# Kernel optimization log

Hardware: AMD Instinct MI355X
Metric: run time of the kernel (lower is better)

Reference implementation:

```python
import jax, jax.numpy as jnp
import numpy as np

# YOLOv2 COCO anchors (w, h) in cell units
ANCHORS = np.array([[0.57273, 0.677385],
                    [1.87446, 2.06253],
                    [3.33843, 5.47434],
                    [7.88282, 3.52778],
                    [9.77052, 9.16828]], dtype=np.float32)

N, S, A, C = 16, 52, 5, 80
L_XY, L_WH, L_OBJ, L_NOOBJ, L_CLS = 5.0, 5.0, 1.0, 0.5, 1.0


def setup_inputs() -> dict:
    key = jax.random.key(0)
    k1, k2 = jax.random.split(key)
    pred = jax.random.normal(k1, (N, S, S, A, 5 + C), dtype=jnp.float32)
    target = jax.random.uniform(k2, (N, S, S, A, 5 + C), dtype=jnp.float32)
    return {"pred": pred, "target": target}


def _pairwise_iou(g, p):
    # g: [..., Agt, 4] gt boxes (cx, cy, w, h); p: [..., Apred, 4]
    g = g[..., :, None, :]   # [..., Agt, 1, 4]
    p = p[..., None, :, :]   # [..., 1, Apred, 4]
    g_x1, g_y1 = g[..., 0] - g[..., 2] / 2, g[..., 1] - g[..., 3] / 2
    g_x2, g_y2 = g[..., 0] + g[..., 2] / 2, g[..., 1] + g[..., 3] / 2
    p_x1, p_y1 = p[..., 0] - p[..., 2] / 2, p[..., 1] - p[..., 3] / 2
    p_x2, p_y2 = p[..., 0] + p[..., 2] / 2, p[..., 1] + p[..., 3] / 2
    iw = jnp.clip(jnp.minimum(g_x2, p_x2) - jnp.maximum(g_x1, p_x1), 0)
    ih = jnp.clip(jnp.minimum(g_y2, p_y2) - jnp.maximum(g_y1, p_y1), 0)
    inter = iw * ih
    union = (g_x2 - g_x1) * (g_y2 - g_y1) + (p_x2 - p_x1) * (p_y2 - p_y1) - inter + 1e-9
    return inter / union  # [..., Agt, Apred]


def reference(pred, target):
    anchors = jnp.asarray(ANCHORS, dtype=pred.dtype)
    aw, ah = anchors[:, 0], anchors[:, 1]  # broadcast over trailing anchor dim

    sx = jax.nn.sigmoid(pred[..., 0])
    sy = jax.nn.sigmoid(pred[..., 1])
    p_tw, p_th, p_to = pred[..., 2], pred[..., 3], pred[..., 4]
    pred_cls = pred[..., 5:]

    # decoded boxes, [N,S,S,A,4]
    p_box = jnp.stack([sx, sy, jnp.exp(p_tw) * aw, jnp.exp(p_th) * ah], axis=-1)
    g_box = jnp.stack([target[..., 0], target[..., 1],
                       jnp.exp(target[..., 2]) * aw,
                       jnp.exp(target[..., 3]) * ah], axis=-1)

    ious = _pairwise_iou(g_box, p_box)  # [N,S,S,Agt,Apred]

    # sequential greedy anchor assignment per cell (A is small and fixed)
    taken = jnp.zeros(pred.shape[:4], dtype=bool)          # [N,S,S,A]
    aligned = jnp.zeros_like(target)                       # [N,S,S,A,5+C]
    ar = jnp.arange(A)
    for a in range(A):
        valid = target[..., a, 4] > 0.5                    # [N,S,S]
        row = jnp.where(taken, -1.0, ious[..., a, :])      # [N,S,S,A]
        best = jnp.argmax(row, axis=-1)                    # [N,S,S]
        sel = (ar == best[..., None]) & valid[..., None]   # [N,S,S,A]
        taken = taken | sel
        aligned = jnp.where(sel[..., None], target[..., a, :][..., None, :], aligned)

    obj = aligned[..., 4] > 0.5                            # [N,S,S,A]
    objf = obj.astype(pred.dtype)

    loss_xy = L_XY * jnp.sum(objf * ((sx - aligned[..., 0]) ** 2 + (sy - aligned[..., 1]) ** 2))
    loss_wh = L_WH * jnp.sum(objf * ((p_tw - aligned[..., 2]) ** 2 + (p_th - aligned[..., 3]) ** 2))
    loss_obj = L_OBJ * jnp.sum(objf * jax.nn.softplus(-p_to))
    loss_noobj = L_NOOBJ * jnp.sum((1.0 - objf) * jax.nn.softplus(p_to))

    logp = jax.nn.log_softmax(pred_cls, axis=-1)
    labels = jnp.argmax(aligned[..., 5:], axis=-1)
    nll = -jnp.take_along_axis(logp, labels[..., None], axis=-1)[..., 0]
    loss_cls = L_CLS * jnp.sum(objf * nll)

    total = (loss_xy + loss_wh + loss_obj + loss_noobj + loss_cls) / pred.shape[0]
    return total
```

## Files before the change

### kernel.cpp

```cpp
#include <hip/hip_runtime.h>
#include <math.h>
#include <stdint.h>


#define NIMG   16
#define NA     5
#define STRIDE 85
#define CELLF  (NA * STRIDE)
#define NCELLS 43264
#define CPB    32
#define BT     256
#define NANCHB (CPB * NA)
#define NB     (NCELLS / CPB)

__device__ __constant__ float AW[5] = {0.57273f, 1.87446f, 3.33843f, 7.88282f, 9.77052f};
__device__ __constant__ float AH[5] = {0.677385f, 2.06253f, 5.47434f, 3.52778f, 9.16828f};

__device__ inline float softplusf(float x) {
    return fmaxf(x, 0.0f) + log1pf(expf(-fabsf(x)));
}
__device__ inline float sigmoidf(float x) { return 1.0f / (1.0f + expf(-x)); }

__global__ __launch_bounds__(BT) void yolo_fused(
    const float* __restrict__ pred, const float* __restrict__ target,
    float* __restrict__ part_ws) {
    __shared__ float s_px1[NANCHB], s_px2[NANCHB], s_py1[NANCHB], s_py2[NANCHB], s_pA[NANCHB];
    __shared__ float s_gx1[NANCHB], s_gx2[NANCHB], s_gy1[NANCHB], s_gy2[NANCHB], s_gA[NANCHB];
    __shared__ float s_gobj[NANCHB];
    __shared__ float s_sx[NANCHB], s_sy[NANCHB], s_ptw[NANCHB], s_pth[NANCHB];
    __shared__ float s_spn[NANCHB], s_spp[NANCHB];
    __shared__ float s_tx[NANCHB], s_ty[NANCHB], s_tw[NANCHB], s_th[NANCHB];
    __shared__ uint32_t s_assign[CPB];
    __shared__ float s_wpart[BT / 64];

    const int t = threadIdx.x;

    if (t < NANCHB) {
        const int ga = blockIdx.x * NANCHB + t;
        const int a = t % NA;
        const float* pa = pred   + (size_t)ga * STRIDE;
        const float* ta = target + (size_t)ga * STRIDE;
        const float p0 = pa[0], p1 = pa[1], p2 = pa[2], p3 = pa[3], p4 = pa[4];
        const float t0 = ta[0], t1 = ta[1], t2 = ta[2], t3 = ta[3], t4 = ta[4];
        const float aw = AW[a], ah = AH[a];

        const float sx = sigmoidf(p0);
        const float sy = sigmoidf(p1);
        const float pw = expf(p2) * aw, ph = expf(p3) * ah;
        const float gw = expf(t2) * aw, gh = expf(t3) * ah;

        s_px1[t] = sx - pw * 0.5f;  s_px2[t] = sx + pw * 0.5f;
        s_py1[t] = sy - ph * 0.5f;  s_py2[t] = sy + ph * 0.5f;
        s_pA[t]  = pw * ph;
        s_gx1[t] = t0 - gw * 0.5f;  s_gx2[t] = t0 + gw * 0.5f;
        s_gy1[t] = t1 - gh * 0.5f;  s_gy2[t] = t1 + gh * 0.5f;
        s_gA[t]  = gw * gh;
        s_gobj[t] = t4;
        s_sx[t] = sx;  s_sy[t] = sy;  s_ptw[t] = p2;  s_pth[t] = p3;
        s_spn[t] = softplusf(-p4);    s_spp[t] = softplusf(p4);
        s_tx[t] = t0;  s_ty[t] = t1;  s_tw[t] = t2;  s_th[t] = t3;
    }
    __syncthreads();

    float loss = 0.0f;
    if (t < CPB) {
        const int la = t * NA;
        float iou[NA][NA];
#pragma unroll
        for (int g = 0; g < NA; ++g) {
            const float gx1 = s_gx1[la+g], gx2 = s_gx2[la+g];
            const float gy1 = s_gy1[la+g], gy2 = s_gy2[la+g];
            const float gA  = s_gA[la+g];
#pragma unroll
            for (int p = 0; p < NA; ++p) {
                float iw = fmaxf(fminf(gx2, s_px2[la+p]) - fmaxf(gx1, s_px1[la+p]), 0.0f);
                float ih = fmaxf(fminf(gy2, s_py2[la+p]) - fmaxf(gy1, s_py1[la+p]), 0.0f);
                float inter = iw * ih;
                iou[g][p] = inter / (gA + s_pA[la+p] - inter + 1e-9f);
            }
        }
        int assign[NA] = {-1, -1, -1, -1, -1};
        bool taken[NA] = {false, false, false, false, false};
#pragma unroll
        for (int g = 0; g < NA; ++g) {
            if (s_gobj[la+g] > 0.5f) {
                float best = -2.0f; int bi = 0;
#pragma unroll
                for (int p = 0; p < NA; ++p) {
                    float v = taken[p] ? -1.0f : iou[g][p];
                    if (v > best) { best = v; bi = p; }
                }
                taken[bi] = true;
                assign[bi] = g;
            }
        }
        uint32_t word = 0;
        float l_xy = 0.f, l_wh = 0.f, l_obj = 0.f, l_noobj = 0.f;
#pragma unroll
        for (int p = 0; p < NA; ++p) {
            const int g = assign[p];
            word |= (uint32_t)(g + 1) << (4 * p);
            if (g >= 0) {
                float dx = s_sx[la+p] - s_tx[la+g];
                float dy = s_sy[la+p] - s_ty[la+g];
                l_xy += dx * dx + dy * dy;
                float dw = s_ptw[la+p] - s_tw[la+g];
                float dh = s_pth[la+p] - s_th[la+g];
                l_wh += dw * dw + dh * dh;
                l_obj += s_spn[la+p];
            } else {
                l_noobj += s_spp[la+p];
            }
        }
        s_assign[t] = word;
        loss = 5.0f * l_xy + 5.0f * l_wh + 1.0f * l_obj + 0.5f * l_noobj;
    }
    __syncthreads();

    const int grp = t >> 4;
    const int ln  = t & 15;
#pragma unroll
    for (int si = 0; si < 10; ++si) {
        const int slot = grp * 10 + si;
        const int cell = slot / NA;
        const int p    = slot - cell * NA;
        const int g    = (int)((s_assign[cell] >> (4 * p)) & 0xFu) - 1;
        if (g >= 0) {
            const size_t cbase = ((size_t)blockIdx.x * CPB + cell) * CELLF;
            const float* pc = pred   + cbase + p * STRIDE + 5;
            const float* tc = target + cbase + g * STRIDE + 5;
            float pv[5], tv[5];
#pragma unroll
            for (int k = 0; k < 5; ++k) {
                pv[k] = pc[ln + 16 * k];
                tv[k] = tc[ln + 16 * k];
            }
            float m = fmaxf(fmaxf(fmaxf(pv[0], pv[1]), fmaxf(pv[2], pv[3])), pv[4]);
#pragma unroll
            for (int o = 1; o < 16; o <<= 1) m = fmaxf(m, __shfl_xor(m, o));
            float s = 0.f;
#pragma unroll
            for (int k = 0; k < 5; ++k) s += expf(pv[k] - m);
#pragma unroll
            for (int o = 1; o < 16; o <<= 1) s += __shfl_xor(s, o);
            float lse = m + logf(s);

            float bt = tv[0]; int bi = ln; float bp = pv[0];
#pragma unroll
            for (int k = 1; k < 5; ++k) {
                if (tv[k] > bt) { bt = tv[k]; bi = ln + 16 * k; bp = pv[k]; }
            }
#pragma unroll
            for (int o = 1; o < 16; o <<= 1) {
                float ot = __shfl_xor(bt, o);
                int   oi = __shfl_xor(bi, o);
                float op = __shfl_xor(bp, o);
                if (ot > bt || (ot == bt && oi < bi)) { bt = ot; bi = oi; bp = op; }
            }
            if (ln == 0) loss += lse - bp;
        }
    }

#pragma unroll
    for (int o = 32; o; o >>= 1) loss += __shfl_xor(loss, o);
    if ((t & 63) == 0) s_wpart[t >> 6] = loss;
    __syncthreads();
    if (t == 0)
        part_ws[blockIdx.x] = s_wpart[0] + s_wpart[1] + s_wpart[2] + s_wpart[3];
}

__global__ __launch_bounds__(256) void yolo_reduce(
    const float* __restrict__ part_ws, float* __restrict__ out) {
    __shared__ float ws4[4];
    float s = 0.0f;
    for (int i = threadIdx.x; i < NB; i += 256) s += part_ws[i];
#pragma unroll
    for (int o = 32; o; o >>= 1) s += __shfl_xor(s, o);
    if ((threadIdx.x & 63) == 0) ws4[threadIdx.x >> 6] = s;
    __syncthreads();
    if (threadIdx.x == 0)
        out[0] = (ws4[0] + ws4[1] + ws4[2] + ws4[3]) * (1.0f / (float)NIMG);
}

extern "C" void kernel_launch(void* const* d_in, const int* in_sizes, int n_in,
                              void* d_out, int out_size, void* d_ws, size_t ws_size,
                              hipStream_t stream) {
    const float* pred   = (const float*)d_in[0];
    const float* target = (const float*)d_in[1];
    float* out = (float*)d_out;
    float* part_ws = (float*)d_ws;

    yolo_fused<<<NB, BT, 0, stream>>>(pred, target, part_ws);
    yolo_reduce<<<1, 256, 0, stream>>>(part_ws, out);
}
```

Before: 170.1 us.

## Stage whole cell blocks into LDS with coalesced float4 loads, shrink cells per block

```diff
diff --git a/kernel.cpp b/kernel.cpp
--- a/kernel.cpp
+++ b/kernel.cpp
@@ -8,9 +8,11 @@
 #define STRIDE 85
 #define CELLF  (NA * STRIDE)
 #define NCELLS 43264
-#define CPB    32
+#define CPB    8
 #define BT     256
 #define NANCHB (CPB * NA)
+#define BLKF   (CPB * CELLF)
+#define BLKV4  (BLKF / 4)
 #define NB     (NCELLS / CPB)
 
 __device__ __constant__ float AW[5] = {0.57273f, 1.87446f, 3.33843f, 7.88282f, 9.77052f};
@@ -24,6 +26,8 @@
 __global__ __launch_bounds__(BT) void yolo_fused(
     const float* __restrict__ pred, const float* __restrict__ target,
     float* __restrict__ part_ws) {
+    __shared__ float4 s_p4[BLKV4];
+    __shared__ float4 s_t4[BLKV4];
     __shared__ float s_px1[NANCHB], s_px2[NANCHB], s_py1[NANCHB], s_py2[NANCHB], s_pA[NANCHB];
     __shared__ float s_gx1[NANCHB], s_gx2[NANCHB], s_gy1[NANCHB], s_gy2[NANCHB], s_gA[NANCHB];
     __shared__ float s_gobj[NANCHB];
@@ -35,30 +39,40 @@
 
     const int t = threadIdx.x;
 
+    const float4* gp = reinterpret_cast<const float4*>(pred   + (size_t)blockIdx.x * BLKF);
+    const float4* gt = reinterpret_cast<const float4*>(target + (size_t)blockIdx.x * BLKF);
+    for (int i = t; i < BLKV4; i += BT) {
+        s_p4[i] = gp[i];
+        s_t4[i] = gt[i];
+    }
+    __syncthreads();
+
+    const float* sp = reinterpret_cast<const float*>(s_p4);
+    const float* st = reinterpret_cast<const float*>(s_t4);
+
     if (t < NANCHB) {
-        const int ga = blockIdx.x * NANCHB + t;
         const int a = t % NA;
-        const float* pa = pred   + (size_t)ga * STRIDE;
-        const float* ta = target + (size_t)ga * STRIDE;
+        const float* pa = sp + t * STRIDE;
         const float p0 = pa[0], p1 = pa[1], p2 = pa[2], p3 = pa[3], p4 = pa[4];
-        const float t0 = ta[0], t1 = ta[1], t2 = ta[2], t3 = ta[3], t4 = ta[4];
-        const float aw = AW[a], ah = AH[a];
-
         const float sx = sigmoidf(p0);
         const float sy = sigmoidf(p1);
-        const float pw = expf(p2) * aw, ph = expf(p3) * ah;
-        const float gw = expf(t2) * aw, gh = expf(t3) * ah;
-
+        const float pw = expf(p2) * AW[a], ph = expf(p3) * AH[a];
         s_px1[t] = sx - pw * 0.5f;  s_px2[t] = sx + pw * 0.5f;
         s_py1[t] = sy - ph * 0.5f;  s_py2[t] = sy + ph * 0.5f;
         s_pA[t]  = pw * ph;
-        s_gx1[t] = t0 - gw * 0.5f;  s_gx2[t] = t0 + gw * 0.5f;
-        s_gy1[t] = t1 - gh * 0.5f;  s_gy2[t] = t1 + gh * 0.5f;
-        s_gA[t]  = gw * gh;
-        s_gobj[t] = t4;
         s_sx[t] = sx;  s_sy[t] = sy;  s_ptw[t] = p2;  s_pth[t] = p3;
-        s_spn[t] = softplusf(-p4);    s_spp[t] = softplusf(p4);
-        s_tx[t] = t0;  s_ty[t] = t1;  s_tw[t] = t2;  s_th[t] = t3;
+        s_spn[t] = softplusf(-p4);   s_spp[t] = softplusf(p4);
+    } else if (t >= 64 && t < 64 + NANCHB) {
+        const int u = t - 64;
+        const int a = u % NA;
+        const float* ta = st + u * STRIDE;
+        const float t0 = ta[0], t1 = ta[1], t2 = ta[2], t3 = ta[3], t4 = ta[4];
+        const float gw = expf(t2) * AW[a], gh = expf(t3) * AH[a];
+        s_gx1[u] = t0 - gw * 0.5f;  s_gx2[u] = t0 + gw * 0.5f;
+        s_gy1[u] = t1 - gh * 0.5f;  s_gy2[u] = t1 + gh * 0.5f;
+        s_gA[u]  = gw * gh;
+        s_gobj[u] = t4;
+        s_tx[u] = t0;  s_ty[u] = t1;  s_tw[u] = t2;  s_th[u] = t3;
     }
     __syncthreads();
 
@@ -120,44 +134,45 @@
     const int grp = t >> 4;
     const int ln  = t & 15;
 #pragma unroll
-    for (int si = 0; si < 10; ++si) {
-        const int slot = grp * 10 + si;
-        const int cell = slot / NA;
-        const int p    = slot - cell * NA;
-        const int g    = (int)((s_assign[cell] >> (4 * p)) & 0xFu) - 1;
-        if (g >= 0) {
-            const size_t cbase = ((size_t)blockIdx.x * CPB + cell) * CELLF;
-            const float* pc = pred   + cbase + p * STRIDE + 5;
-            const float* tc = target + cbase + g * STRIDE + 5;
-            float pv[5], tv[5];
-#pragma unroll
-            for (int k = 0; k < 5; ++k) {
-                pv[k] = pc[ln + 16 * k];
-                tv[k] = tc[ln + 16 * k];
-            }
-            float m = fmaxf(fmaxf(fmaxf(pv[0], pv[1]), fmaxf(pv[2], pv[3])), pv[4]);
-#pragma unroll
-            for (int o = 1; o < 16; o <<= 1) m = fmaxf(m, __shfl_xor(m, o));
-            float s = 0.f;
-#pragma unroll
-            for (int k = 0; k < 5; ++k) s += expf(pv[k] - m);
-#pragma unroll
-            for (int o = 1; o < 16; o <<= 1) s += __shfl_xor(s, o);
-            float lse = m + logf(s);
-
-            float bt = tv[0]; int bi = ln; float bp = pv[0];
-#pragma unroll
-            for (int k = 1; k < 5; ++k) {
-                if (tv[k] > bt) { bt = tv[k]; bi = ln + 16 * k; bp = pv[k]; }
-            }
-#pragma unroll
-            for (int o = 1; o < 16; o <<= 1) {
-                float ot = __shfl_xor(bt, o);
-                int   oi = __shfl_xor(bi, o);
-                float op = __shfl_xor(bp, o);
-                if (ot > bt || (ot == bt && oi < bi)) { bt = ot; bi = oi; bp = op; }
-            }
-            if (ln == 0) loss += lse - bp;
+    for (int r = 0; r < 3; ++r) {
+        const int slot = r * 16 + grp;
+        if (slot < NANCHB) {
+            const int cell = slot / NA;
+            const int p    = slot - cell * NA;
+            const int g    = (int)((s_assign[cell] >> (4 * p)) & 0xFu) - 1;
+            if (g >= 0) {
+                const float* pc = sp + cell * CELLF + p * STRIDE + 5;
+                const float* tc = st + cell * CELLF + g * STRIDE + 5;
+                float pv[5], tv[5];
+#pragma unroll
+                for (int k = 0; k < 5; ++k) {
+                    pv[k] = pc[ln + 16 * k];
+                    tv[k] = tc[ln + 16 * k];
+                }
+                float m = fmaxf(fmaxf(fmaxf(pv[0], pv[1]), fmaxf(pv[2], pv[3])), pv[4]);
+#pragma unroll
+                for (int o = 1; o < 16; o <<= 1) m = fmaxf(m, __shfl_xor(m, o));
+                float s = 0.f;
+#pragma unroll
+                for (int k = 0; k < 5; ++k) s += expf(pv[k] - m);
+#pragma unroll
+                for (int o = 1; o < 16; o <<= 1) s += __shfl_xor(s, o);
+                float lse = m + logf(s);
+
+                float bt = tv[0]; int bi = ln; float bp = pv[0];
+#pragma unroll
+                for (int k = 1; k < 5; ++k) {
+                    if (tv[k] > bt) { bt = tv[k]; bi = ln + 16 * k; bp = pv[k]; }
+                }
+#pragma unroll
+                for (int o = 1; o < 16; o <<= 1) {
+                    float ot = __shfl_xor(bt, o);
+                    int   oi = __shfl_xor(bi, o);
+                    float op = __shfl_xor(bp, o);
+                    if (ot > bt || (ot == bt && oi < bi)) { bt = ot; bi = oi; bp = op; }
+                }
+                if (ln == 0) loss += lse - bp;
+            }
         }
     }
 
```

Result: slower. 199.6 us (+17.3%).
